# Performance work log

Measured on AMD Instinct MI355X. Metric: run time of the kernel, lower is better.

Reference implementation:

```python
import jax, jax.numpy as jnp
import numpy as np

N, LQ, C, NH, NL, NP, DFFN = 8, 900, 256, 8, 4, 4, 1024
SHAPES = [(128, 128), (64, 64), (32, 32), (16, 16)]
LEN = sum(h * w for h, w in SHAPES)


def _ln(x, g, b):
    m = jnp.mean(x, -1, keepdims=True)
    v = jnp.var(x, -1, keepdims=True)
    return (x - m) / jnp.sqrt(v + 1e-5) * g + b


def _mha(q, k, v, w_qkv, b_qkv, w_o, b_o):
    # torch nn.MultiheadAttention with packed in_proj; batch-first layout here (same math)
    d = q.shape[-1]
    dh = d // NH
    qp = q @ w_qkv[:d].T + b_qkv[:d]
    kp = k @ w_qkv[d:2 * d].T + b_qkv[d:2 * d]
    vp = v @ w_qkv[2 * d:].T + b_qkv[2 * d:]
    qh = qp.reshape(*q.shape[:2], NH, dh)
    kh = kp.reshape(*k.shape[:2], NH, dh)
    vh = vp.reshape(*v.shape[:2], NH, dh)
    logits = jnp.einsum('bqhd,bkhd->bhqk', qh, kh) / jnp.sqrt(jnp.asarray(dh, qh.dtype))
    attn = jax.nn.softmax(logits, -1)
    o = jnp.einsum('bhqk,bkhd->bqhd', attn, vh).reshape(*q.shape[:2], d)
    return o @ w_o.T + b_o


def _msdeform(query, ref, src, shapes, pad_mask, w_v, b_v, w_off, b_off, w_a, b_a, w_o, b_o):
    n, length, d = src.shape
    lq = query.shape[1]
    dh = d // NH
    value = src @ w_v.T + b_v
    value = jnp.where(pad_mask[..., None], 0.0, value)
    vt = value.reshape(n, length, NH, dh).transpose(0, 2, 1, 3)  # (N,NH,Len,Dh)
    off = (query @ w_off.T + b_off).reshape(n, lq, NH, NL, NP, 2)
    a = (query @ w_a.T + b_a).reshape(n, lq, NH, NL * NP)
    a = jax.nn.softmax(a, -1).reshape(n, lq, NH, NL, NP)
    norm = jnp.asarray([[w, h] for (h, w) in shapes], dtype=query.dtype)  # (NL,2) as (W,H)
    loc = ref[:, :, None, :, None, :] + off / norm[None, None, None, :, None, :]
    loc = loc.transpose(0, 2, 1, 3, 4, 5)  # (N,NH,Lq,NL,NP,2)
    a_t = a.transpose(0, 2, 1, 3, 4)       # (N,NH,Lq,NL,NP)
    out = jnp.zeros((n, NH, lq, dh), query.dtype)
    start = 0
    for l, (hs, ws) in enumerate(shapes):
        hs, ws = int(hs), int(ws)
        vl = vt[:, :, start:start + hs * ws]
        start += hs * ws
        # grid_sample align_corners=False, zero padding
        x = loc[:, :, :, l, :, 0] * ws - 0.5
        y = loc[:, :, :, l, :, 1] * hs - 0.5
        x0, y0 = jnp.floor(x), jnp.floor(y)
        wx, wy = x - x0, y - y0

        def g(xi, yi):
            valid = (xi >= 0) & (xi < ws) & (yi >= 0) & (yi < hs)
            idx = (jnp.clip(yi, 0, hs - 1) * ws + jnp.clip(xi, 0, ws - 1)).astype(jnp.int32)
            gat = jnp.take_along_axis(vl, idx.reshape(n, NH, -1)[..., None], axis=2)
            return gat.reshape(n, NH, lq, NP, dh) * valid[..., None].astype(vl.dtype)

        s = (((1 - wx) * (1 - wy))[..., None] * g(x0, y0)
             + (wx * (1 - wy))[..., None] * g(x0 + 1, y0)
             + ((1 - wx) * wy)[..., None] * g(x0, y0 + 1)
             + (wx * wy)[..., None] * g(x0 + 1, y0 + 1))
        out = out + jnp.sum(s * a_t[:, :, :, l, :, None], axis=3)
    out = out.transpose(0, 2, 1, 3).reshape(n, lq, d)
    return out @ w_o.T + b_o


def setup_inputs() -> dict:
    key = jax.random.key(0)
    ks = jax.random.split(key, 24)
    w = lambda k, *s: (jax.random.normal(k, s, jnp.float32) * 0.02)
    inp = {
        'tgt': jax.random.normal(ks[0], (N, LQ, C), jnp.float32),
        'query_pos': jax.random.normal(ks[1], (N, LQ, C), jnp.float32),
        'reference_points': jax.random.uniform(ks[2], (N, LQ, NL, 2), jnp.float32),
        'src': jax.random.normal(ks[3], (N, LEN, C), jnp.float32),
        'src_spatial_shapes': jnp.asarray(SHAPES, jnp.int64),
        'level_start_index': jnp.asarray(np.cumsum([0] + [h * w for h, w in SHAPES[:-1]]), jnp.int64),
        'src_padding_mask': jnp.zeros((N, LEN), bool),
        # self-attn params
        'sa_in_w': w(ks[4], 3 * C, C), 'sa_in_b': jnp.zeros((3 * C,), jnp.float32),
        'sa_out_w': w(ks[5], C, C), 'sa_out_b': jnp.zeros((C,), jnp.float32),
        # MSDeformAttn params
        'ca_off_w': w(ks[6], NH * NL * NP * 2, C), 'ca_off_b': w(ks[7], NH * NL * NP * 2) * 5.0,
        'ca_aw_w': w(ks[8], NH * NL * NP, C), 'ca_aw_b': jnp.zeros((NH * NL * NP,), jnp.float32),
        'ca_val_w': w(ks[9], C, C), 'ca_val_b': jnp.zeros((C,), jnp.float32),
        'ca_out_w': w(ks[10], C, C), 'ca_out_b': jnp.zeros((C,), jnp.float32),
        # layer norms
        'n1_g': 1.0 + w(ks[11], C), 'n1_b': w(ks[12], C),
        'n2_g': 1.0 + w(ks[13], C), 'n2_b': w(ks[14], C),
        'n3_g': 1.0 + w(ks[15], C), 'n3_b': w(ks[16], C),
        # FFN
        'f1_w': w(ks[17], DFFN, C), 'f1_b': jnp.zeros((DFFN,), jnp.float32),
        'f2_w': w(ks[18], C, DFFN), 'f2_b': jnp.zeros((C,), jnp.float32),
    }
    return inp


def reference(tgt, query_pos, reference_points, src, src_spatial_shapes, level_start_index,
              src_padding_mask, sa_in_w, sa_in_b, sa_out_w, sa_out_b, ca_off_w, ca_off_b,
              ca_aw_w, ca_aw_b, ca_val_w, ca_val_b, ca_out_w, ca_out_b, n1_g, n1_b, n2_g, n2_b,
              n3_g, n3_b, f1_w, f1_b, f2_w, f2_b):
    shapes = np.asarray(src_spatial_shapes)
    # self-attention (data_domain_type='src_only' path), eval mode -> dropout identity
    q = tgt + query_pos
    tgt2 = _mha(q, q, tgt, sa_in_w, sa_in_b, sa_out_w, sa_out_b)
    tgt = _ln(tgt + tgt2, n2_g, n2_b)
    # multi-scale deformable cross-attention
    tgt2 = _msdeform(tgt + query_pos, reference_points, src, shapes, src_padding_mask,
                     ca_val_w, ca_val_b, ca_off_w, ca_off_b, ca_aw_w, ca_aw_b, ca_out_w, ca_out_b)
    tgt = _ln(tgt + tgt2, n1_g, n1_b)
    # FFN
    tgt2 = jax.nn.relu(tgt @ f1_w.T + f1_b) @ f2_w.T + f2_b
    return _ln(tgt + tgt2, n3_g, n3_b)
```

## Files before the change

kernel.cpp:

```cpp
#include <hip/hip_runtime.h>
#include <cstdint>

constexpr int NB   = 8;
constexpr int LQn  = 900;
constexpr int CD   = 256;
constexpr int LENS = 21760;
constexpr int NQ   = NB * LQn;
constexpr int NV   = NB * LENS;

using short8 = __attribute__((ext_vector_type(8))) short;
using f32x4  = __attribute__((ext_vector_type(4))) float;

__device__ __forceinline__ ushort f2b(float x) {
    uint32_t u = __builtin_bit_cast(uint32_t, x);
    u += 0x7fffu + ((u >> 16) & 1u);
    return (ushort)(u >> 16);
}
__device__ __forceinline__ float b2f(ushort x) {
    uint32_t u = ((uint32_t)x) << 16;
    return __builtin_bit_cast(float, u);
}
__device__ __forceinline__ float b2f_lo(uint32_t u) {
    return __builtin_bit_cast(float, u << 16);
}
__device__ __forceinline__ float b2f_hi(uint32_t u) {
    return __builtin_bit_cast(float, u & 0xffff0000u);
}

struct WPtrs { const float* p[8]; };
__constant__ const int kWOff[9] = {0, 196608, 262144, 327680, 360448, 425984,
                                   491520, 753664, 1015808};

__global__ __launch_bounds__(256) void cvt_w_kernel(
    WPtrs w, ushort* __restrict__ out,
    const float* __restrict__ offb, const float* __restrict__ awb,
    float* __restrict__ biascat)
{
    if (blockIdx.x == 992) {
        int t = threadIdx.x;
        if (t < 384) biascat[t] = t < 256 ? offb[t] : awb[t - 256];
        return;
    }
    int i = blockIdx.x * blockDim.x + threadIdx.x;
    int e = i * 4;
    int s = 0;
#pragma unroll
    for (int k = 1; k < 8; ++k) if (e >= kWOff[k]) s = k;
    float4 v = *reinterpret_cast<const float4*>(w.p[s] + (e - kWOff[s]));
    ushort4 o;
    o.x = f2b(v.x); o.y = f2b(v.y); o.z = f2b(v.z); o.w = f2b(v.w);
    *reinterpret_cast<ushort4*>(out + e) = o;
}

__global__ __launch_bounds__(256) void cvt_pair_kernel(
    const float* __restrict__ a, const float* __restrict__ b,
    ushort* __restrict__ sum_bf, ushort* __restrict__ a_bf, int n4) {
    int i = blockIdx.x * blockDim.x + threadIdx.x;
    if (i >= n4) return;
    float4 va = reinterpret_cast<const float4*>(a)[i];
    float4 vb = reinterpret_cast<const float4*>(b)[i];
    ushort4 s, t;
    s.x = f2b(va.x + vb.x); s.y = f2b(va.y + vb.y);
    s.z = f2b(va.z + vb.z); s.w = f2b(va.w + vb.w);
    reinterpret_cast<ushort4*>(sum_bf)[i] = s;
    t.x = f2b(va.x); t.y = f2b(va.y); t.z = f2b(va.z); t.w = f2b(va.w);
    reinterpret_cast<ushort4*>(a_bf)[i] = t;
}

template<int BM, bool A_F32, int OUTK, bool RELU, bool MASK>
__global__ __launch_bounds__(256) void gemm_mfma(
    const void* __restrict__ Av, const ushort* __restrict__ B,
    const float* __restrict__ bias, void* __restrict__ Cv,
    int M, int K, int ldc, const unsigned char* __restrict__ rowmask)
{
    constexpr int RIT = BM / 64;
    constexpr int FR  = BM / 32;
    __shared__ ushort As[BM * 32];
    __shared__ ushort Bs[4096];

    const int tid = threadIdx.x, lane = tid & 63, wave = tid >> 6;
    const int wr = wave >> 1, wc = wave & 1;
    const int bn = blockIdx.x * 128;
    const int bm = blockIdx.y * BM;
    const int lc15 = lane & 15, lk = lane >> 4;

    f32x4 acc[FR][4] = {};

    int a_off[FR], b_off[4];
#pragma unroll
    for (int fr = 0; fr < FR; ++fr) {
        int r = wr * (BM / 2) + fr * 16 + lc15;
        a_off[fr] = r * 32 + ((lk ^ ((r >> 1) & 3)) * 8);
    }
#pragma unroll
    for (int fc = 0; fc < 4; ++fc) {
        int rb = wc * 64 + fc * 16 + lc15;
        b_off[fc] = rb * 32 + ((lk ^ ((rb >> 1) & 3)) * 8);
    }

    for (int k0 = 0; k0 < K; k0 += 32) {
        if constexpr (!A_F32) {
            const ushort* A = (const ushort*)Av;
#pragma unroll
            for (int t = 0; t < RIT; ++t) {
                int row = wave * (16 * RIT) + t * 16 + (lane >> 2);
                int p = lane & 3;
                int g = p ^ ((row >> 1) & 3);
                size_t ar = (size_t)bm + row; if (ar >= (size_t)M) ar = M - 1;
                const ushort* gp = A + ar * (size_t)K + k0 + g * 8;
                __builtin_amdgcn_global_load_lds(
                    (const __attribute__((address_space(1))) uint32_t*)gp,
                    (__attribute__((address_space(3))) uint32_t*)(As + (wave * RIT + t) * 512),
                    16, 0, 0);
            }
        } else {
            const float* A = (const float*)Av;
#pragma unroll
            for (int t = 0; t < RIT; ++t) {
                int s = tid + t * 256;
                int row = s >> 2, p = s & 3;
                int g = p ^ ((row >> 1) & 3);
                size_t ar = (size_t)bm + row; if (ar >= (size_t)M) ar = M - 1;
                const float* gp = A + ar * (size_t)K + k0 + g * 8;
                float4 v0 = *reinterpret_cast<const float4*>(gp);
                float4 v1 = *reinterpret_cast<const float4*>(gp + 4);
                short8 pk;
                pk[0] = (short)f2b(v0.x); pk[1] = (short)f2b(v0.y);
                pk[2] = (short)f2b(v0.z); pk[3] = (short)f2b(v0.w);
                pk[4] = (short)f2b(v1.x); pk[5] = (short)f2b(v1.y);
                pk[6] = (short)f2b(v1.z); pk[7] = (short)f2b(v1.w);
                *reinterpret_cast<short8*>(&As[row * 32 + p * 8]) = pk;
            }
        }
        {
#pragma unroll
            for (int t = 0; t < 2; ++t) {
                int row = wave * 32 + t * 16 + (lane >> 2);
                int p = lane & 3;
                int g = p ^ ((row >> 1) & 3);
                const ushort* gp = B + (size_t)(bn + row) * K + k0 + g * 8;
                __builtin_amdgcn_global_load_lds(
                    (const __attribute__((address_space(1))) uint32_t*)gp,
                    (__attribute__((address_space(3))) uint32_t*)(Bs + (wave * 2 + t) * 512),
                    16, 0, 0);
            }
        }
        __syncthreads();

        short8 af[FR], bfr[4];
#pragma unroll
        for (int fr = 0; fr < FR; ++fr) af[fr]  = *reinterpret_cast<const short8*>(&As[a_off[fr]]);
#pragma unroll
        for (int fc = 0; fc < 4; ++fc) bfr[fc] = *reinterpret_cast<const short8*>(&Bs[b_off[fc]]);
#pragma unroll
        for (int fr = 0; fr < FR; ++fr)
#pragma unroll
            for (int fc = 0; fc < 4; ++fc)
                acc[fr][fc] = __builtin_amdgcn_mfma_f32_16x16x32_bf16(
                    af[fr], bfr[fc], acc[fr][fc], 0, 0, 0);
        __syncthreads();
    }

#pragma unroll
    for (int fc = 0; fc < 4; ++fc) {
        int col = bn + wc * 64 + fc * 16 + lc15;
        float bv = bias[col];
#pragma unroll
        for (int fr = 0; fr < FR; ++fr) {
            int rb = bm + wr * (BM / 2) + fr * 16 + lk * 4;
#pragma unroll
            for (int r = 0; r < 4; ++r) {
                int row = rb + r;
                if (row < M) {
                    float v = acc[fr][fc][r] + bv;
                    if constexpr (RELU) v = fmaxf(v, 0.f);
                    if constexpr (MASK) { if (rowmask[row]) v = 0.f; }
                    if constexpr (OUTK == 0)
                        ((float*)Cv)[(size_t)row * ldc + col] = v;
                    else if constexpr (OUTK == 1)
                        ((ushort*)Cv)[(size_t)row * ldc + col] = f2b(v);
                    else {
                        int brow = row / LENS;
                        int len  = row - brow * LENS;
                        int hh = col >> 5, ch = col & 31;
                        ((ushort*)Cv)[((size_t)(brow * 8 + hh) * LENS + len) * 32 + ch] = f2b(v);
                    }
                }
            }
        }
    }
}

__global__ __launch_bounds__(256) void attn_mfma(
    const ushort* __restrict__ qkv, ushort* __restrict__ out)
{
    __shared__ ushort Vt[32][72];
    __shared__ ushort Plds[4][16][72];

    const int tid = threadIdx.x, lane = tid & 63, wave = tid >> 6;
    const int lq = lane & 15, lg = lane >> 4;
    const int q0 = blockIdx.x * 64;
    const int h = blockIdx.y, b = blockIdx.z;
    const size_t bbase = (size_t)b * LQn * 768;

    int qrow = q0 + wave * 16 + lq; if (qrow > LQn - 1) qrow = LQn - 1;
    short8 aq = *reinterpret_cast<const short8*>(
        qkv + bbase + (size_t)qrow * 768 + h * 32 + lg * 8);

    f32x4 accO[2] = {};
    float m[4], l[4];
#pragma unroll
    for (int r = 0; r < 4; ++r) { m[r] = -3.0e38f; l[r] = 0.f; }

    for (int kt = 0; kt < 15; ++kt) {
        const int kb = kt * 64;
        __syncthreads();
        {
            int key = tid >> 2, dhc = (tid & 3) * 8;
            int kg = kb + key; if (kg > LQn - 1) kg = LQn - 1;
            short8 vv = *reinterpret_cast<const short8*>(
                qkv + bbase + (size_t)kg * 768 + 512 + h * 32 + dhc);
#pragma unroll
            for (int j = 0; j < 8; ++j) Vt[dhc + j][key] = (ushort)vv[j];
        }
        __syncthreads();

        f32x4 s4[4];
#pragma unroll
        for (int fc = 0; fc < 4; ++fc) {
            int krow = kb + fc * 16 + lq;
            int kc = krow > LQn - 1 ? LQn - 1 : krow;
            short8 bk = *reinterpret_cast<const short8*>(
                qkv + bbase + (size_t)kc * 768 + 256 + h * 32 + lg * 8);
            f32x4 z = {};
            s4[fc] = __builtin_amdgcn_mfma_f32_16x16x32_bf16(aq, bk, z, 0, 0, 0);
            bool inval = krow >= LQn;
#pragma unroll
            for (int r = 0; r < 4; ++r)
                s4[fc][r] = inval ? -3.0e38f : s4[fc][r] * 0.17677669529663687f;
        }

#pragma unroll
        for (int r = 0; r < 4; ++r) {
            float rm = fmaxf(fmaxf(s4[0][r], s4[1][r]), fmaxf(s4[2][r], s4[3][r]));
            rm = fmaxf(rm, __shfl_xor(rm, 1));
            rm = fmaxf(rm, __shfl_xor(rm, 2));
            rm = fmaxf(rm, __shfl_xor(rm, 4));
            rm = fmaxf(rm, __shfl_xor(rm, 8));
            float mn = fmaxf(m[r], rm);
            float esc = __expf(m[r] - mn);
            float rs = 0.f;
#pragma unroll
            for (int fc = 0; fc < 4; ++fc) {
                float p = __expf(s4[fc][r] - mn);
                s4[fc][r] = p; rs += p;
            }
            rs += __shfl_xor(rs, 1); rs += __shfl_xor(rs, 2);
            rs += __shfl_xor(rs, 4); rs += __shfl_xor(rs, 8);
            m[r] = mn;
            l[r] = l[r] * esc + rs;
            accO[0][r] *= esc; accO[1][r] *= esc;
        }

#pragma unroll
        for (int fc = 0; fc < 4; ++fc)
#pragma unroll
            for (int r = 0; r < 4; ++r)
                Plds[wave][lg * 4 + r][fc * 16 + lq] = f2b(s4[fc][r]);

#pragma unroll
        for (int ks = 0; ks < 2; ++ks) {
            short8 ap = *reinterpret_cast<const short8*>(&Plds[wave][lq][ks * 32 + lg * 8]);
#pragma unroll
            for (int fc = 0; fc < 2; ++fc) {
                short8 bv = *reinterpret_cast<const short8*>(&Vt[fc * 16 + lq][ks * 32 + lg * 8]);
                accO[fc] = __builtin_amdgcn_mfma_f32_16x16x32_bf16(ap, bv, accO[fc], 0, 0, 0);
            }
        }
    }

#pragma unroll
    for (int r = 0; r < 4; ++r) {
        int q = q0 + wave * 16 + lg * 4 + r;
        if (q < LQn) {
            float invl = 1.f / l[r];
#pragma unroll
            for (int fc = 0; fc < 2; ++fc)
                out[((size_t)b * LQn + q) * 256 + h * 32 + fc * 16 + lq] =
                    f2b(accO[fc][r] * invl);
        }
    }
}

__global__ __launch_bounds__(256) void deform2_kernel(
    const ushort* __restrict__ valt,
    const float* __restrict__ offaw,
    const float* __restrict__ ref,
    ushort* __restrict__ out)
{
    __shared__ int   Pi[16][16][4];
    __shared__ float Pw[16][16][4];

    const int tid = threadIdx.x;
    const int grp = tid >> 4;
    const int lane = tid & 15;
    const int gg = blockIdx.x * 16 + grp;
    const int h  = gg / 7200;
    const int bq = gg - h * 7200;
    const int b  = bq / LQn;

    const float* row = offaw + (size_t)bq * 384;
    float aval = row[256 + h * 16 + lane];
    float mx = aval;
    mx = fmaxf(mx, __shfl_xor(mx, 1));
    mx = fmaxf(mx, __shfl_xor(mx, 2));
    mx = fmaxf(mx, __shfl_xor(mx, 4));
    mx = fmaxf(mx, __shfl_xor(mx, 8));
    float e = __expf(aval - mx);
    float se = e;
    se += __shfl_xor(se, 1); se += __shfl_xor(se, 2);
    se += __shfl_xor(se, 4); se += __shfl_xor(se, 8);
    float a = e / se;

    const int lv = lane >> 2;
    const int W = 128 >> lv;
    const int STl[4] = {0, 16384, 20480, 21504};
    const float Wf = (float)W;
    float2 off2 = *reinterpret_cast<const float2*>(row + h * 32 + lane * 2);
    float rx = ref[(size_t)bq * 8 + lv * 2];
    float ry = ref[(size_t)bq * 8 + lv * 2 + 1];
    float x = (rx + off2.x / Wf) * Wf - 0.5f;
    float y = (ry + off2.y / Wf) * Wf - 0.5f;
    float x0f = floorf(x), y0f = floorf(y);
    int x0 = (int)x0f, y0 = (int)y0f;
    float wx = x - x0f, wy = y - y0f;
    float vx0 = (x0 >= 0 && x0 < W) ? 1.f : 0.f;
    float vx1 = (x0 + 1 >= 0 && x0 + 1 < W) ? 1.f : 0.f;
    float vy0 = (y0 >= 0 && y0 < W) ? 1.f : 0.f;
    float vy1 = (y0 + 1 >= 0 && y0 + 1 < W) ? 1.f : 0.f;
    int x0c = min(max(x0, 0), W - 1), x1c = min(max(x0 + 1, 0), W - 1);
    int y0c = min(max(y0, 0), W - 1), y1c = min(max(y0 + 1, 0), W - 1);
    int base = STl[lv];
    Pi[grp][lane][0] = base + y0c * W + x0c;
    Pi[grp][lane][1] = base + y0c * W + x1c;
    Pi[grp][lane][2] = base + y1c * W + x0c;
    Pi[grp][lane][3] = base + y1c * W + x1c;
    Pw[grp][lane][0] = (1.f - wx) * (1.f - wy) * vx0 * vy0 * a;
    Pw[grp][lane][1] = wx * (1.f - wy) * vx1 * vy0 * a;
    Pw[grp][lane][2] = (1.f - wx) * wy * vx0 * vy1 * a;
    Pw[grp][lane][3] = wx * wy * vx1 * vy1 * a;

    const ushort* vb = valt + (size_t)(b * 8 + h) * (LENS * 32);
    float accx = 0.f, accy = 0.f;
#pragma unroll 4
    for (int s = 0; s < 16; ++s) {
        int4  idx = *reinterpret_cast<const int4*>(Pi[grp][s]);
        float4 w  = *reinterpret_cast<const float4*>(Pw[grp][s]);
        uint32_t u00 = *reinterpret_cast<const uint32_t*>(vb + idx.x * 32 + lane * 2);
        uint32_t u10 = *reinterpret_cast<const uint32_t*>(vb + idx.y * 32 + lane * 2);
        uint32_t u01 = *reinterpret_cast<const uint32_t*>(vb + idx.z * 32 + lane * 2);
        uint32_t u11 = *reinterpret_cast<const uint32_t*>(vb + idx.w * 32 + lane * 2);
        accx = fmaf(w.x, b2f_lo(u00), accx); accy = fmaf(w.x, b2f_hi(u00), accy);
        accx = fmaf(w.y, b2f_lo(u10), accx); accy = fmaf(w.y, b2f_hi(u10), accy);
        accx = fmaf(w.z, b2f_lo(u01), accx); accy = fmaf(w.z, b2f_hi(u01), accy);
        accx = fmaf(w.w, b2f_lo(u11), accx); accy = fmaf(w.w, b2f_hi(u11), accy);
    }
    uint32_t pack = ((uint32_t)f2b(accy) << 16) | (uint32_t)f2b(accx);
    *reinterpret_cast<uint32_t*>(out + (size_t)bq * 256 + h * 32 + lane * 2) = pack;
}

__global__ __launch_bounds__(256) void ln_kernel(
    const float* __restrict__ x, const float* __restrict__ y,
    const float* __restrict__ g, const float* __restrict__ beta,
    float* __restrict__ out, ushort* __restrict__ out_bf,
    const float* __restrict__ qpos, ushort* __restrict__ qadd_bf)
{
    const int r = blockIdx.x;
    const int c = threadIdx.x;
    float v = x[(size_t)r * 256 + c] + y[(size_t)r * 256 + c];
    float s1 = v, s2 = v * v;
#pragma unroll
    for (int msk = 32; msk; msk >>= 1) {
        s1 += __shfl_xor(s1, msk);
        s2 += __shfl_xor(s2, msk);
    }
    __shared__ float red[8];
    int w = c >> 6;
    if ((c & 63) == 0) { red[w] = s1; red[4 + w] = s2; }
    __syncthreads();
    s1 = red[0] + red[1] + red[2] + red[3];
    s2 = red[4] + red[5] + red[6] + red[7];
    float mean = s1 * (1.f / 256.f);
    float var  = s2 * (1.f / 256.f) - mean * mean;
    float inv  = 1.f / sqrtf(var + 1e-5f);
    float o = (v - mean) * inv * g[c] + beta[c];
    out[(size_t)r * 256 + c] = o;
    if (out_bf) out_bf[(size_t)r * 256 + c] = f2b(o);
    if (qadd_bf) qadd_bf[(size_t)r * 256 + c] = f2b(o + qpos[(size_t)r * 256 + c]);
}

extern "C" void kernel_launch(void* const* d_in, const int* in_sizes, int n_in,
                              void* d_out, int out_size, void* d_ws, size_t ws_size,
                              hipStream_t stream)
{
    const float* tgt      = (const float*)d_in[0];
    const float* qpos     = (const float*)d_in[1];
    const float* refpts   = (const float*)d_in[2];
    const float* src      = (const float*)d_in[3];
    const unsigned char* padmask = (const unsigned char*)d_in[6];
    const float* sa_in_w  = (const float*)d_in[7];
    const float* sa_in_b  = (const float*)d_in[8];
    const float* sa_out_w = (const float*)d_in[9];
    const float* sa_out_b = (const float*)d_in[10];
    const float* ca_off_w = (const float*)d_in[11];
    const float* ca_off_b = (const float*)d_in[12];
    const float* ca_aw_w  = (const float*)d_in[13];
    const float* ca_aw_b  = (const float*)d_in[14];
    const float* ca_val_w = (const float*)d_in[15];
    const float* ca_val_b = (const float*)d_in[16];
    const float* ca_out_w = (const float*)d_in[17];
    const float* ca_out_b = (const float*)d_in[18];
    const float* n1_g     = (const float*)d_in[19];
    const float* n1_b     = (const float*)d_in[20];
    const float* n2_g     = (const float*)d_in[21];
    const float* n2_b     = (const float*)d_in[22];
    const float* n3_g     = (const float*)d_in[23];
    const float* n3_b     = (const float*)d_in[24];
    const float* f1_w     = (const float*)d_in[25];
    const float* f1_b     = (const float*)d_in[26];
    const float* f2_w     = (const float*)d_in[27];
    const float* f2_b     = (const float*)d_in[28];
    float* out = (float*)d_out;
    (void)in_sizes; (void)n_in; (void)out_size; (void)ws_size;

    float* ws = (float*)d_ws;
    size_t fo = 0;
    auto fa = [&](size_t n) { float* p = ws + fo; fo += n; return p; };
    float* buf_p   = fa((size_t)NQ * 256);
    float* t1      = fa((size_t)NQ * 256);
    float* t2      = fa((size_t)NQ * 256);
    float* offaw   = fa((size_t)NQ * 384);
    float* biascat = fa(384);
    fo = (fo + 3) & ~(size_t)3;
    ushort* ub = (ushort*)(ws + fo);
    size_t uo = 0;
    auto ua = [&](size_t n) { ushort* p = ub + uo; uo += n; return p; };
    ushort* w_bf    = ua(1015808);
    ushort* q_bf    = ua((size_t)NQ * 256);
    ushort* tgt_bf  = ua((size_t)NQ * 256);
    ushort* q2_bf   = ua((size_t)NQ * 256);
    ushort* qkv_bf  = ua((size_t)NQ * 768);
    ushort* attn_bf = ua((size_t)NQ * 256);
    ushort* dfo_bf  = ua((size_t)NQ * 256);
    ushort* t2_bf   = ua((size_t)NQ * 256);
    ushort* hid_bf  = ua((size_t)NQ * 1024);
    ushort* val_t   = ua((size_t)NV * 256);

    const ushort* w_sa_in  = w_bf + 0;
    const ushort* w_sa_out = w_bf + 196608;
    const ushort* w_offaw  = w_bf + 262144;
    const ushort* w_ca_val = w_bf + 360448;
    const ushort* w_ca_out = w_bf + 425984;
    const ushort* w_f1     = w_bf + 491520;
    const ushort* w_f2     = w_bf + 753664;

    dim3 blk(256);
    const int n4 = NQ * 256 / 4;

    WPtrs wp;
    wp.p[0] = sa_in_w; wp.p[1] = sa_out_w; wp.p[2] = ca_off_w; wp.p[3] = ca_aw_w;
    wp.p[4] = ca_val_w; wp.p[5] = ca_out_w; wp.p[6] = f1_w; wp.p[7] = f2_w;
    cvt_w_kernel<<<993, blk, 0, stream>>>(wp, w_bf, ca_off_b, ca_aw_b, biascat);

    cvt_pair_kernel<<<1800, blk, 0, stream>>>(tgt, qpos, q_bf, tgt_bf, n4);
    gemm_mfma<64, false, 1, false, false><<<dim3(4, 113), blk, 0, stream>>>(
        q_bf, w_sa_in, sa_in_b, qkv_bf, NQ, 256, 768, nullptr);
    gemm_mfma<64, false, 1, false, false><<<dim3(2, 113), blk, 0, stream>>>(
        tgt_bf, w_sa_in + 512 * 256, sa_in_b + 512, qkv_bf + 512, NQ, 256, 768, nullptr);
    attn_mfma<<<dim3(15, 8, 8), blk, 0, stream>>>(qkv_bf, attn_bf);
    gemm_mfma<64, false, 0, false, false><<<dim3(2, 113), blk, 0, stream>>>(
        attn_bf, w_sa_out, sa_out_b, buf_p, NQ, 256, 256, nullptr);
    ln_kernel<<<NQ, blk, 0, stream>>>(tgt, buf_p, n2_g, n2_b, t1, nullptr, qpos, q2_bf);

    gemm_mfma<128, true, 2, false, true><<<dim3(2, 1360), blk, 0, stream>>>(
        src, w_ca_val, ca_val_b, val_t, NV, 256, 256, padmask);
    gemm_mfma<64, false, 0, false, false><<<dim3(3, 113), blk, 0, stream>>>(
        q2_bf, w_offaw, biascat, offaw, NQ, 256, 384, nullptr);
    deform2_kernel<<<3600, blk, 0, stream>>>(val_t, offaw, refpts, dfo_bf);
    gemm_mfma<64, false, 0, false, false><<<dim3(2, 113), blk, 0, stream>>>(
        dfo_bf, w_ca_out, ca_out_b, buf_p, NQ, 256, 256, nullptr);
    ln_kernel<<<NQ, blk, 0, stream>>>(t1, buf_p, n1_g, n1_b, t2, t2_bf, nullptr, nullptr);

    gemm_mfma<128, false, 1, true, false><<<dim3(8, 57), blk, 0, stream>>>(
        t2_bf, w_f1, f1_b, hid_bf, NQ, 256, 1024, nullptr);
    gemm_mfma<64, false, 0, false, false><<<dim3(2, 113), blk, 0, stream>>>(
        hid_bf, w_f2, f2_b, buf_p, NQ, 1024, 256, nullptr);
    ln_kernel<<<NQ, blk, 0, stream>>>(t2, buf_p, n3_g, n3_b, out, nullptr, nullptr, nullptr);
}
```

Measured before the change: 582.6 us.

## Double-buffer LDS tiles in GEMM and prefetch K/V in attention

The MFMA GEMM now uses two LDS buffers per operand and issues the next k-tile's global loads before computing the current tile. This removes one barrier per iteration and overlaps memory latency with MFMA work. The fp32-A path keeps the prefetched values in registers and packs them with v_cvt_pk_bf16_f32. Self-attention prefetches the next K/V tile into registers and double-buffers the transposed V in LDS. The cost is twice the LDS and more live registers, which may reduce occupancy.

```diff
diff --git a/kernel.cpp b/kernel.cpp
--- a/kernel.cpp
+++ b/kernel.cpp
@@ -26,6 +26,11 @@
 __device__ __forceinline__ float b2f_hi(uint32_t u) {
     return __builtin_bit_cast(float, u & 0xffff0000u);
 }
+__device__ __forceinline__ uint32_t cvtpk(float lo, float hi) {
+    uint32_t r;
+    asm("v_cvt_pk_bf16_f32 %0, %1, %2" : "=v"(r) : "v"(lo), "v"(hi));
+    return r;
+}
 
 struct WPtrs { const float* p[8]; };
 __constant__ const int kWOff[9] = {0, 196608, 262144, 327680, 360448, 425984,
@@ -37,8 +42,8 @@
     float* __restrict__ biascat)
 {
     if (blockIdx.x == 992) {
-        int t = threadIdx.x;
-        if (t < 384) biascat[t] = t < 256 ? offb[t] : awb[t - 256];
+        for (int t = threadIdx.x; t < 384; t += 256)
+            biascat[t] = t < 256 ? offb[t] : awb[t - 256];
         return;
     }
     int i = blockIdx.x * blockDim.x + threadIdx.x;
@@ -75,8 +80,8 @@
 {
     constexpr int RIT = BM / 64;
     constexpr int FR  = BM / 32;
-    __shared__ ushort As[BM * 32];
-    __shared__ ushort Bs[4096];
+    __shared__ ushort As[2][BM * 32];
+    __shared__ ushort Bs[2][4096];
 
     const int tid = threadIdx.x, lane = tid & 63, wave = tid >> 6;
     const int wr = wave >> 1, wc = wave & 1;
@@ -84,6 +89,9 @@
     const int bm = blockIdx.y * BM;
     const int lc15 = lane & 15, lk = lane >> 4;
 
+    const ushort* Abf = (const ushort*)Av;
+    const float*  Afp = (const float*)Av;
+
     f32x4 acc[FR][4] = {};
 
     int a_off[FR], b_off[4];
@@ -98,67 +106,95 @@
         b_off[fc] = rb * 32 + ((lk ^ ((rb >> 1) & 3)) * 8);
     }
 
-    for (int k0 = 0; k0 < K; k0 += 32) {
-        if constexpr (!A_F32) {
-            const ushort* A = (const ushort*)Av;
-#pragma unroll
-            for (int t = 0; t < RIT; ++t) {
-                int row = wave * (16 * RIT) + t * 16 + (lane >> 2);
-                int p = lane & 3;
-                int g = p ^ ((row >> 1) & 3);
-                size_t ar = (size_t)bm + row; if (ar >= (size_t)M) ar = M - 1;
-                const ushort* gp = A + ar * (size_t)K + k0 + g * 8;
-                __builtin_amdgcn_global_load_lds(
-                    (const __attribute__((address_space(1))) uint32_t*)gp,
-                    (__attribute__((address_space(3))) uint32_t*)(As + (wave * RIT + t) * 512),
-                    16, 0, 0);
-            }
+    float4 pa0[RIT], pa1[RIT];
+
+    auto loadA_regs = [&](int k0) {
+#pragma unroll
+        for (int t = 0; t < RIT; ++t) {
+            int s = tid + t * 256;
+            int row = s >> 2, p = s & 3;
+            int g = p ^ ((row >> 1) & 3);
+            size_t ar = (size_t)bm + row; if (ar >= (size_t)M) ar = M - 1;
+            const float* gp = Afp + ar * (size_t)K + k0 + g * 8;
+            pa0[t] = *reinterpret_cast<const float4*>(gp);
+            pa1[t] = *reinterpret_cast<const float4*>(gp + 4);
+        }
+    };
+    auto writeA_lds = [&](int buf) {
+#pragma unroll
+        for (int t = 0; t < RIT; ++t) {
+            int s = tid + t * 256;
+            int row = s >> 2, p = s & 3;
+            uint4 pk;
+            pk.x = cvtpk(pa0[t].x, pa0[t].y);
+            pk.y = cvtpk(pa0[t].z, pa0[t].w);
+            pk.z = cvtpk(pa1[t].x, pa1[t].y);
+            pk.w = cvtpk(pa1[t].z, pa1[t].w);
+            *reinterpret_cast<uint4*>(&As[buf][row * 32 + p * 8]) = pk;
+        }
+    };
+    auto stageA_lds = [&](int buf, int k0) {
+#pragma unroll
+        for (int t = 0; t < RIT; ++t) {
+            int row = wave * (16 * RIT) + t * 16 + (lane >> 2);
+            int p = lane & 3;
+            int g = p ^ ((row >> 1) & 3);
+            size_t ar = (size_t)bm + row; if (ar >= (size_t)M) ar = M - 1;
+            const ushort* gp = Abf + ar * (size_t)K + k0 + g * 8;
+            __builtin_amdgcn_global_load_lds(
+                (const __attribute__((address_space(1))) uint32_t*)gp,
+                (__attribute__((address_space(3))) uint32_t*)(&As[buf][(wave * RIT + t) * 512]),
+                16, 0, 0);
+        }
+    };
+    auto stageB = [&](int buf, int k0) {
+#pragma unroll
+        for (int t = 0; t < 2; ++t) {
+            int row = wave * 32 + t * 16 + (lane >> 2);
+            int p = lane & 3;
+            int g = p ^ ((row >> 1) & 3);
+            const ushort* gp = B + (size_t)(bn + row) * K + k0 + g * 8;
+            __builtin_amdgcn_global_load_lds(
+                (const __attribute__((address_space(1))) uint32_t*)gp,
+                (__attribute__((address_space(3))) uint32_t*)(&Bs[buf][(wave * 2 + t) * 512]),
+                16, 0, 0);
+        }
+    };
+
+    if constexpr (A_F32) { loadA_regs(0); writeA_lds(0); }
+    else stageA_lds(0, 0);
+    stageB(0, 0);
+    __syncthreads();
+
+    const int nt = K >> 5;
+    int cur = 0;
+    for (int t = 0; t < nt; ++t) {
+        const int k0n = (t + 1) << 5;
+        const bool more = (t + 1 < nt);
+        if constexpr (A_F32) {
+            if (more) loadA_regs(k0n);
         } else {
-            const float* A = (const float*)Av;
-#pragma unroll
-            for (int t = 0; t < RIT; ++t) {
-                int s = tid + t * 256;
-                int row = s >> 2, p = s & 3;
-                int g = p ^ ((row >> 1) & 3);
-                size_t ar = (size_t)bm + row; if (ar >= (size_t)M) ar = M - 1;
-                const float* gp = A + ar * (size_t)K + k0 + g * 8;
-                float4 v0 = *reinterpret_cast<const float4*>(gp);
-                float4 v1 = *reinterpret_cast<const float4*>(gp + 4);
-                short8 pk;
-                pk[0] = (short)f2b(v0.x); pk[1] = (short)f2b(v0.y);
-                pk[2] = (short)f2b(v0.z); pk[3] = (short)f2b(v0.w);
-                pk[4] = (short)f2b(v1.x); pk[5] = (short)f2b(v1.y);
-                pk[6] = (short)f2b(v1.z); pk[7] = (short)f2b(v1.w);
-                *reinterpret_cast<short8*>(&As[row * 32 + p * 8]) = pk;
-            }
-        }
-        {
-#pragma unroll
-            for (int t = 0; t < 2; ++t) {
-                int row = wave * 32 + t * 16 + (lane >> 2);
-                int p = lane & 3;
-                int g = p ^ ((row >> 1) & 3);
-                const ushort* gp = B + (size_t)(bn + row) * K + k0 + g * 8;
-                __builtin_amdgcn_global_load_lds(
-                    (const __attribute__((address_space(1))) uint32_t*)gp,
-                    (__attribute__((address_space(3))) uint32_t*)(Bs + (wave * 2 + t) * 512),
-                    16, 0, 0);
-            }
-        }
-        __syncthreads();
+            if (more) stageA_lds(cur ^ 1, k0n);
+        }
+        if (more) stageB(cur ^ 1, k0n);
 
         short8 af[FR], bfr[4];
 #pragma unroll
-        for (int fr = 0; fr < FR; ++fr) af[fr]  = *reinterpret_cast<const short8*>(&As[a_off[fr]]);
-#pragma unroll
-        for (int fc = 0; fc < 4; ++fc) bfr[fc] = *reinterpret_cast<const short8*>(&Bs[b_off[fc]]);
+        for (int fr = 0; fr < FR; ++fr) af[fr]  = *reinterpret_cast<const short8*>(&As[cur][a_off[fr]]);
+#pragma unroll
+        for (int fc = 0; fc < 4; ++fc) bfr[fc] = *reinterpret_cast<const short8*>(&Bs[cur][b_off[fc]]);
 #pragma unroll
         for (int fr = 0; fr < FR; ++fr)
 #pragma unroll
             for (int fc = 0; fc < 4; ++fc)
                 acc[fr][fc] = __builtin_amdgcn_mfma_f32_16x16x32_bf16(
                     af[fr], bfr[fc], acc[fr][fc], 0, 0, 0);
+
+        if constexpr (A_F32) {
+            if (more) writeA_lds(cur ^ 1);
+        }
         __syncthreads();
+        cur ^= 1;
     }
 
 #pragma unroll
@@ -194,7 +230,7 @@
 __global__ __launch_bounds__(256) void attn_mfma(
     const ushort* __restrict__ qkv, ushort* __restrict__ out)
 {
-    __shared__ ushort Vt[32][72];
+    __shared__ ushort Vt[2][32][72];
     __shared__ ushort Plds[4][16][72];
 
     const int tid = threadIdx.x, lane = tid & 63, wave = tid >> 6;
@@ -207,33 +243,49 @@
     short8 aq = *reinterpret_cast<const short8*>(
         qkv + bbase + (size_t)qrow * 768 + h * 32 + lg * 8);
 
-    f32x4 accO[2] = {};
-    float m[4], l[4];
-#pragma unroll
-    for (int r = 0; r < 4; ++r) { m[r] = -3.0e38f; l[r] = 0.f; }
-
-    for (int kt = 0; kt < 15; ++kt) {
-        const int kb = kt * 64;
-        __syncthreads();
-        {
-            int key = tid >> 2, dhc = (tid & 3) * 8;
-            int kg = kb + key; if (kg > LQn - 1) kg = LQn - 1;
-            short8 vv = *reinterpret_cast<const short8*>(
-                qkv + bbase + (size_t)kg * 768 + 512 + h * 32 + dhc);
-#pragma unroll
-            for (int j = 0; j < 8; ++j) Vt[dhc + j][key] = (ushort)vv[j];
-        }
-        __syncthreads();
-
-        f32x4 s4[4];
+    const int vkey = tid >> 2, vdhc = (tid & 3) * 8;
+
+    auto loadV = [&](int kb) {
+        int kg = kb + vkey; if (kg > LQn - 1) kg = LQn - 1;
+        return *reinterpret_cast<const short8*>(
+            qkv + bbase + (size_t)kg * 768 + 512 + h * 32 + vdhc);
+    };
+    auto loadK = [&](int kb, short8* bk) {
 #pragma unroll
         for (int fc = 0; fc < 4; ++fc) {
             int krow = kb + fc * 16 + lq;
             int kc = krow > LQn - 1 ? LQn - 1 : krow;
-            short8 bk = *reinterpret_cast<const short8*>(
+            bk[fc] = *reinterpret_cast<const short8*>(
                 qkv + bbase + (size_t)kc * 768 + 256 + h * 32 + lg * 8);
+        }
+    };
+
+    f32x4 accO[2] = {};
+    float m[4], l[4];
+#pragma unroll
+    for (int r = 0; r < 4; ++r) { m[r] = -3.0e38f; l[r] = 0.f; }
+
+    short8 vreg = loadV(0);
+    short8 kreg[4]; loadK(0, kreg);
+
+    int cur = 0;
+    for (int kt = 0; kt < 15; ++kt) {
+        const int kb = kt * 64;
+#pragma unroll
+        for (int j = 0; j < 8; ++j) Vt[cur][vdhc + j][vkey] = (ushort)vreg[j];
+        __syncthreads();
+
+        f32x4 s4[4];
+#pragma unroll
+        for (int fc = 0; fc < 4; ++fc) {
             f32x4 z = {};
-            s4[fc] = __builtin_amdgcn_mfma_f32_16x16x32_bf16(aq, bk, z, 0, 0, 0);
+            s4[fc] = __builtin_amdgcn_mfma_f32_16x16x32_bf16(aq, kreg[fc], z, 0, 0, 0);
+        }
+        if (kt + 1 < 15) { vreg = loadV(kb + 64); loadK(kb + 64, kreg); }
+
+#pragma unroll
+        for (int fc = 0; fc < 4; ++fc) {
+            int krow = kb + fc * 16 + lq;
             bool inval = krow >= LQn;
 #pragma unroll
             for (int r = 0; r < 4; ++r)
@@ -273,10 +325,11 @@
             short8 ap = *reinterpret_cast<const short8*>(&Plds[wave][lq][ks * 32 + lg * 8]);
 #pragma unroll
             for (int fc = 0; fc < 2; ++fc) {
-                short8 bv = *reinterpret_cast<const short8*>(&Vt[fc * 16 + lq][ks * 32 + lg * 8]);
+                short8 bv = *reinterpret_cast<const short8*>(&Vt[cur][fc * 16 + lq][ks * 32 + lg * 8]);
                 accO[fc] = __builtin_amdgcn_mfma_f32_16x16x32_bf16(ap, bv, accO[fc], 0, 0, 0);
             }
         }
+        cur ^= 1;
     }
 
 #pragma unroll
```

Result: no change. 574.4 us (-1.4%).
